# Performance work log

Measured on AMD Instinct MI355X. Metric: run time of the kernel, lower is better.

The kernel has to match this reference:

```python
import jax, jax.numpy as jnp
import numpy as np

BS, GRID, LSTM_H, CNN_C, PROJ = 256, 49, 512, 2048, 512


def setup_inputs() -> dict:
    key = jax.random.key(0)
    ks = jax.random.split(key, 7)
    s = lambda fan_in: 1.0 / np.sqrt(fan_in)
    return {
        "lstm_hidden": jax.random.normal(ks[0], (BS, LSTM_H), jnp.float32),
        "cnn_feat": jax.random.normal(ks[1], (BS, GRID, CNN_C), jnp.float32),
        "W_lstm": jax.random.normal(ks[2], (PROJ, LSTM_H), jnp.float32) * s(LSTM_H),
        "b_lstm": jax.random.normal(ks[3], (PROJ,), jnp.float32) * s(LSTM_H),
        "W_cnn": jax.random.normal(ks[4], (PROJ, CNN_C), jnp.float32) * s(CNN_C),
        "b_cnn": jax.random.normal(ks[5], (PROJ,), jnp.float32) * s(CNN_C),
        "w_attn": jax.random.normal(ks[6], (1, PROJ), jnp.float32) * s(PROJ),
    }


def reference(lstm_hidden, cnn_feat, W_lstm, b_lstm, W_cnn, b_cnn, w_attn):
    # H computed once (original loop recomputes it per grid, identically)
    H = lstm_hidden @ W_lstm.T + b_lstm                       # (bs, P)
    V = jnp.einsum("bgc,pc->bgp", cnn_feat, W_cnn) + b_cnn    # (bs, G, P)
    z = jnp.tanh(H[:, None, :] + V) @ w_attn[0]               # (bs, G)
    bs, G = z.shape
    # Faithful to torch: cat over grids along dim 0 -> (G*bs,), then view(bs, G)
    z_scrambled = jnp.swapaxes(z, 0, 1).reshape(bs, G)
    return jax.nn.softmax(z_scrambled, axis=1)
```

## Files before the change

kernel.cpp:

```cpp
#include <hip/hip_runtime.h>
#include <math.h>

#define BSZ    256
#define GRID_N 49
#define LSTMH  512
#define CNN_C  2048
#define PROJ   512
#define KAUG   2560
#define M_TOT  12544
#define MT     64
#define NT     128
#define BK     64
#define KTILES (KAUG / BK)
#define NBLK   ((M_TOT / MT) * (PROJ / NT))

typedef short bf16x8 __attribute__((ext_vector_type(8)));
typedef float f32x4  __attribute__((ext_vector_type(4)));

static __device__ __forceinline__ unsigned short bf16_rne(float f) {
    unsigned int u = __float_as_uint(f);
    u = u + 0x7FFFu + ((u >> 16) & 1u);
    return (unsigned short)(u >> 16);
}
static __device__ __forceinline__ uint4 pack8f(const float* f) {
    uint4 o;
    o.x = (unsigned int)bf16_rne(f[0]) | ((unsigned int)bf16_rne(f[1]) << 16);
    o.y = (unsigned int)bf16_rne(f[2]) | ((unsigned int)bf16_rne(f[3]) << 16);
    o.z = (unsigned int)bf16_rne(f[4]) | ((unsigned int)bf16_rne(f[5]) << 16);
    o.w = (unsigned int)bf16_rne(f[6]) | ((unsigned int)bf16_rne(f[7]) << 16);
    return o;
}
static __device__ __forceinline__ float tanh_fast(float x) {
    float e = __expf(2.f * x);
    return 1.f - 2.f / (e + 1.f);
}
static __device__ __forceinline__ void glds16(const void* g, void* l) {
    __builtin_amdgcn_global_load_lds(
        (const __attribute__((address_space(1))) unsigned int*)g,
        (__attribute__((address_space(3))) unsigned int*)l, 16, 0, 0);
}

__global__ __launch_bounds__(256) void prep_w(const float* __restrict__ Wc,
                                              const float* __restrict__ Wl,
                                              unsigned short* __restrict__ wsW) {
    int c  = blockIdx.x * 256 + threadIdx.x;
    int p  = c / 320;
    int kc = (c % 320) * 8;
    const float* src = (kc < CNN_C) ? (Wc + (size_t)p * CNN_C + kc)
                                    : (Wl + (size_t)p * LSTMH + (kc - CNN_C));
    float f[8];
    *(float4*)&f[0] = ((const float4*)src)[0];
    *(float4*)&f[4] = ((const float4*)src)[1];
    *(uint4*)(wsW + (size_t)p * KAUG + kc) = pack8f(f);
}

template <bool WS>
__global__ __launch_bounds__(256, 4) void gemm_k(
    const float* __restrict__ lstm, const float* __restrict__ cnn,
    const float* __restrict__ Wc,   const float* __restrict__ Wl,
    const float* __restrict__ bl,   const float* __restrict__ bc,
    const float* __restrict__ wat,  const unsigned short* __restrict__ wsW,
    float* __restrict__ out)
{
    __shared__ unsigned short Ash[MT][BK];
    __shared__ unsigned short Bsh[NT][BK];
    __shared__ float zp[4][MT];

    const int t   = threadIdx.x;
    const int w   = t >> 6;
    const int l   = t & 63;
    const int q   = l >> 4;
    const int r16 = l & 15;

    const int bid = (int)blockIdx.x;
    const int swz = (bid & 7) * (NBLK / 8) + (bid >> 3);
    const int m0 = (swz >> 2) * MT;
    const int n0 = (swz & 3) * NT;

    const int ra  = t >> 2;
    const int ca0 = t & 3;
    const int sa  = ra & 7;
    const int grow = m0 + ra;
    const int ab   = grow / 49;
    const int ag   = grow - ab * 49;
    const float* cnnb  = cnn + ((size_t)ab * GRID_N + ag) * CNN_C;
    const float* lstmb = lstm + (size_t)ab * LSTMH;

    f32x4 acc[4][2];
    #pragma unroll
    for (int mt = 0; mt < 4; ++mt)
        #pragma unroll
        for (int nt = 0; nt < 2; ++nt)
            acc[mt][nt] = (f32x4){0.f, 0.f, 0.f, 0.f};

    float4 fa0, fa1, fa2, fa3;

    auto a_load = [&](int k0) {
        const float* s = (k0 < CNN_C) ? (cnnb + k0) : (lstmb + (k0 - CNN_C));
        const float4* p0 = (const float4*)(s + ca0 * 8);
        const float4* p1 = (const float4*)(s + (ca0 + 4) * 8);
        fa0 = p0[0]; fa1 = p0[1];
        fa2 = p1[0]; fa3 = p1[1];
    };
    auto a_write = [&]() {
        float f[8];
        *(float4*)&f[0] = fa0; *(float4*)&f[4] = fa1;
        *(uint4*)&Ash[ra][(ca0 ^ sa) * 8] = pack8f(f);
        *(float4*)&f[0] = fa2; *(float4*)&f[4] = fa3;
        *(uint4*)&Ash[ra][((ca0 + 4) ^ sa) * 8] = pack8f(f);
    };
    auto b_stage = [&](int k0) {
        if constexpr (WS) {
            const int rsub = l >> 3;
            const int cg   = (l & 7) ^ rsub;
            #pragma unroll
            for (int j = 0; j < 4; ++j) {
                const int rowb = w * 32 + j * 8;
                const unsigned short* g =
                    wsW + (size_t)(n0 + rowb + rsub) * KAUG + k0 + cg * 8;
                glds16(g, &Bsh[rowb][0]);
            }
        } else {
            const int rb = t >> 1;
            const int hb = t & 1;
            const float* s = (k0 < CNN_C) ? (Wc + (size_t)(n0 + rb) * CNN_C + k0)
                                          : (Wl + (size_t)(n0 + rb) * LSTMH + (k0 - CNN_C));
            const int sw = rb & 7;
            #pragma unroll
            for (int c = 0; c < 4; ++c) {
                const int cc = hb * 4 + c;
                float f[8];
                *(float4*)&f[0] = ((const float4*)(s + cc * 8))[0];
                *(float4*)&f[4] = ((const float4*)(s + cc * 8))[1];
                *(uint4*)&Bsh[rb][(cc ^ sw) * 8] = pack8f(f);
            }
        }
    };

    a_load(0);
    a_write();
    b_stage(0);

    for (int kt = 0; kt < KTILES; ++kt) {
        __syncthreads();
        const bool more = (kt + 1 < KTILES);
        if (more) a_load((kt + 1) * BK);
        #pragma unroll
        for (int ks = 0; ks < 2; ++ks) {
            const int cp = ((ks * 4 + q) ^ (r16 & 7)) * 8;
            bf16x8 af[4], bfr[2];
            #pragma unroll
            for (int mt = 0; mt < 4; ++mt)
                af[mt] = *(const bf16x8*)&Ash[mt * 16 + r16][cp];
            #pragma unroll
            for (int nt = 0; nt < 2; ++nt)
                bfr[nt] = *(const bf16x8*)&Bsh[w * 32 + nt * 16 + r16][cp];
            #pragma unroll
            for (int mt = 0; mt < 4; ++mt)
                #pragma unroll
                for (int nt = 0; nt < 2; ++nt)
                    acc[mt][nt] = __builtin_amdgcn_mfma_f32_16x16x32_bf16(
                        af[mt], bfr[nt], acc[mt][nt], 0, 0, 0);
        }
        __syncthreads();
        if (more) { a_write(); b_stage((kt + 1) * BK); }
    }

    float part[4][4];
    #pragma unroll
    for (int mt = 0; mt < 4; ++mt)
        #pragma unroll
        for (int rr = 0; rr < 4; ++rr) part[mt][rr] = 0.f;
    #pragma unroll
    for (int nt = 0; nt < 2; ++nt) {
        const int p = n0 + w * 32 + nt * 16 + r16;
        const float bb = bl[p] + bc[p];
        const float wa = wat[p];
        #pragma unroll
        for (int mt = 0; mt < 4; ++mt)
            #pragma unroll
            for (int rr = 0; rr < 4; ++rr)
                part[mt][rr] += tanh_fast(acc[mt][nt][rr] + bb) * wa;
    }
    #pragma unroll
    for (int mt = 0; mt < 4; ++mt)
        #pragma unroll
        for (int rr = 0; rr < 4; ++rr) {
            float v = part[mt][rr];
            v += __shfl_xor(v, 1);
            v += __shfl_xor(v, 2);
            v += __shfl_xor(v, 4);
            v += __shfl_xor(v, 8);
            if (r16 == 0) zp[w][mt * 16 + q * 4 + rr] = v;
        }
    __syncthreads();
    if (t < MT) {
        const float v = zp[0][t] + zp[1][t] + zp[2][t] + zp[3][t];
        const int row = m0 + t;
        const int b2  = row / 49;
        const int g2  = row - b2 * 49;
        atomicAdd(&out[g2 * BSZ + b2], v);
    }
}

__global__ __launch_bounds__(64) void softmax_rows(float* __restrict__ out)
{
    const int i = blockIdx.x;
    const int j = threadIdx.x;
    float x = (j < GRID_N) ? out[i * GRID_N + j] : -1e30f;
    float m = x;
    #pragma unroll
    for (int off = 32; off > 0; off >>= 1) m = fmaxf(m, __shfl_xor(m, off));
    float e = (j < GRID_N) ? __expf(x - m) : 0.f;
    float s = e;
    #pragma unroll
    for (int off = 32; off > 0; off >>= 1) s += __shfl_xor(s, off);
    if (j < GRID_N) out[i * GRID_N + j] = e / s;
}

extern "C" void kernel_launch(void* const* d_in, const int* in_sizes, int n_in,
                              void* d_out, int out_size, void* d_ws, size_t ws_size,
                              hipStream_t stream)
{
    const float* lstm = (const float*)d_in[0];
    const float* cnn  = (const float*)d_in[1];
    const float* Wl   = (const float*)d_in[2];
    const float* bl   = (const float*)d_in[3];
    const float* Wc   = (const float*)d_in[4];
    const float* bc   = (const float*)d_in[5];
    const float* wat  = (const float*)d_in[6];
    float* out = (float*)d_out;

    hipMemsetAsync(out, 0, (size_t)out_size * sizeof(float), stream);

    const size_t wneed = (size_t)PROJ * KAUG * sizeof(unsigned short);
    if (ws_size >= wneed) {
        unsigned short* wsW = (unsigned short*)d_ws;
        prep_w<<<dim3(640), dim3(256), 0, stream>>>(Wc, Wl, wsW);
        gemm_k<true><<<dim3(NBLK), dim3(256), 0, stream>>>(lstm, cnn, Wc, Wl, bl, bc, wat, wsW, out);
    } else {
        gemm_k<false><<<dim3(NBLK), dim3(256), 0, stream>>>(lstm, cnn, Wc, Wl, bl, bc, wat, nullptr, out);
    }
    softmax_rows<<<dim3(BSZ), dim3(64), 0, stream>>>(out);
}
```

Baseline: 246.6 us.

## Pre-convert activations to bf16 and use a 128x128 double-buffered direct-to-LDS GEMM

A new prep kernel converts cnn_feat and lstm_hidden to bf16 in workspace alongside the weights, and also zeroes the output, which removes the separate memset. A new GEMM kernel uses 128x128 tiles with double-buffered LDS filled through global_load_lds for both operands. Register-staged fp32 loads and per-tile conversion inside the main loop go away, and each block gets more reuse per tile. The cost is an extra full pass over the 100MB activation tensor, which is read, written as bf16 and read again, and the new path only runs if the workspace is large enough.

```diff
diff --git a/kernel.cpp b/kernel.cpp
--- a/kernel.cpp
+++ b/kernel.cpp
@@ -8,11 +8,22 @@
 #define PROJ   512
 #define KAUG   2560
 #define M_TOT  12544
+#define BK     64
+#define KTILES (KAUG / BK)
+
 #define MT     64
 #define NT     128
-#define BK     64
-#define KTILES (KAUG / BK)
 #define NBLK   ((M_TOT / MT) * (PROJ / NT))
+
+#define MT2    128
+#define NT2    128
+#define NBLK2  ((M_TOT / MT2) * (PROJ / NT2))
+
+#define ACHUNKS (M_TOT * CNN_C / 8)
+#define LCHUNKS (BSZ * LSTMH / 8)
+#define ABLK    ((ACHUNKS + LCHUNKS) / 256)
+#define WBLK    640
+#define PBLK    (ABLK + WBLK)
 
 typedef short bf16x8 __attribute__((ext_vector_type(8)));
 typedef float f32x4  __attribute__((ext_vector_type(4)));
@@ -38,6 +49,161 @@
     __builtin_amdgcn_global_load_lds(
         (const __attribute__((address_space(1))) unsigned int*)g,
         (__attribute__((address_space(3))) unsigned int*)l, 16, 0, 0);
+}
+
+__global__ __launch_bounds__(256) void prep_all(
+    const float* __restrict__ cnn, const float* __restrict__ lstm,
+    const float* __restrict__ Wc,  const float* __restrict__ Wl,
+    unsigned short* __restrict__ wsW, unsigned short* __restrict__ wsA,
+    unsigned short* __restrict__ wsL, float* __restrict__ out)
+{
+    const int bid = blockIdx.x, t = threadIdx.x;
+    if (bid < 49) out[bid * 256 + t] = 0.f;
+    float f[8];
+    if (bid < ABLK) {
+        const int c = bid * 256 + t;
+        const float* src; unsigned short* dst;
+        if (c < ACHUNKS) { src = cnn  + (size_t)c * 8; dst = wsA + (size_t)c * 8; }
+        else { const int c2 = c - ACHUNKS; src = lstm + (size_t)c2 * 8; dst = wsL + (size_t)c2 * 8; }
+        *(float4*)&f[0] = ((const float4*)src)[0];
+        *(float4*)&f[4] = ((const float4*)src)[1];
+        *(uint4*)dst = pack8f(f);
+    } else {
+        const int c  = (bid - ABLK) * 256 + t;
+        const int p  = c / 320;
+        const int kc = (c % 320) * 8;
+        const float* src = (kc < CNN_C) ? (Wc + (size_t)p * CNN_C + kc)
+                                        : (Wl + (size_t)p * LSTMH + (kc - CNN_C));
+        *(float4*)&f[0] = ((const float4*)src)[0];
+        *(float4*)&f[4] = ((const float4*)src)[1];
+        *(uint4*)(wsW + (size_t)p * KAUG + kc) = pack8f(f);
+    }
+}
+
+__global__ __launch_bounds__(256, 2) void gemm2(
+    const unsigned short* __restrict__ wsW, const unsigned short* __restrict__ wsA,
+    const unsigned short* __restrict__ wsL,
+    const float* __restrict__ bl, const float* __restrict__ bc,
+    const float* __restrict__ wat, float* __restrict__ out)
+{
+    __shared__ unsigned short Ab[2][MT2][BK];
+    __shared__ unsigned short Bb[2][NT2][BK];
+
+    const int t   = threadIdx.x;
+    const int w   = t >> 6;
+    const int l   = t & 63;
+    const int q   = l >> 4;
+    const int r16 = l & 15;
+    const int wr  = w >> 1;
+    const int wc  = w & 1;
+
+    const int bid = (int)blockIdx.x;
+    const int swz = (bid & 7) * (NBLK2 / 8) + (bid >> 3);
+    const int m0  = (swz >> 2) * MT2;
+    const int n0  = (swz & 3) * NT2;
+
+    const int srow = l >> 3;
+    const int cg   = (l & 7) ^ srow;
+
+    auto stage = [&](int kt, int bufi) {
+        const int k0 = kt * BK;
+        #pragma unroll
+        for (int jj = 0; jj < 4; ++jj) {
+            const int rowb = w * 32 + jj * 8;
+            const unsigned short* g = wsW + (size_t)(n0 + rowb + srow) * KAUG + k0 + cg * 8;
+            glds16(g, &Bb[bufi][rowb][0]);
+        }
+        if (k0 < CNN_C) {
+            #pragma unroll
+            for (int jj = 0; jj < 4; ++jj) {
+                const int rowa = w * 32 + jj * 8;
+                const unsigned short* g = wsA + (size_t)(m0 + rowa + srow) * CNN_C + k0 + cg * 8;
+                glds16(g, &Ab[bufi][rowa][0]);
+            }
+        } else {
+            const int k0l = k0 - CNN_C;
+            #pragma unroll
+            for (int jj = 0; jj < 4; ++jj) {
+                const int rowa = w * 32 + jj * 8;
+                const int rg   = m0 + rowa + srow;
+                const unsigned short* g = wsL + (size_t)(rg / 49) * LSTMH + k0l + cg * 8;
+                glds16(g, &Ab[bufi][rowa][0]);
+            }
+        }
+    };
+
+    f32x4 acc[4][4];
+    #pragma unroll
+    for (int mt = 0; mt < 4; ++mt)
+        #pragma unroll
+        for (int nt = 0; nt < 4; ++nt)
+            acc[mt][nt] = (f32x4){0.f, 0.f, 0.f, 0.f};
+
+    stage(0, 0);
+    asm volatile("s_waitcnt vmcnt(0)" ::: "memory");
+    __builtin_amdgcn_s_barrier();
+
+    int cur = 0;
+    for (int kt = 0; kt < KTILES; ++kt) {
+        if (kt + 1 < KTILES) stage(kt + 1, cur ^ 1);
+        #pragma unroll
+        for (int ks = 0; ks < 2; ++ks) {
+            const int cp = ((ks * 4 + q) ^ (r16 & 7)) * 8;
+            bf16x8 af[4], bfr[4];
+            #pragma unroll
+            for (int mt = 0; mt < 4; ++mt)
+                af[mt] = *(const bf16x8*)&Ab[cur][wr * 64 + mt * 16 + r16][cp];
+            #pragma unroll
+            for (int nt = 0; nt < 4; ++nt)
+                bfr[nt] = *(const bf16x8*)&Bb[cur][wc * 64 + nt * 16 + r16][cp];
+            #pragma unroll
+            for (int mt = 0; mt < 4; ++mt)
+                #pragma unroll
+                for (int nt = 0; nt < 4; ++nt)
+                    acc[mt][nt] = __builtin_amdgcn_mfma_f32_16x16x32_bf16(
+                        af[mt], bfr[nt], acc[mt][nt], 0, 0, 0);
+        }
+        asm volatile("s_waitcnt vmcnt(0)" ::: "memory");
+        __builtin_amdgcn_s_barrier();
+        cur ^= 1;
+    }
+
+    float* zpf = (float*)&Ab[0][0][0];
+    float part[4][4];
+    #pragma unroll
+    for (int mt = 0; mt < 4; ++mt)
+        #pragma unroll
+        for (int rr = 0; rr < 4; ++rr) part[mt][rr] = 0.f;
+    #pragma unroll
+    for (int nt = 0; nt < 4; ++nt) {
+        const int p = n0 + wc * 64 + nt * 16 + r16;
+        const float bb = bl[p] + bc[p];
+        const float wa = wat[p];
+        #pragma unroll
+        for (int mt = 0; mt < 4; ++mt)
+            #pragma unroll
+            for (int rr = 0; rr < 4; ++rr)
+                part[mt][rr] += tanh_fast(acc[mt][nt][rr] + bb) * wa;
+    }
+    #pragma unroll
+    for (int mt = 0; mt < 4; ++mt)
+        #pragma unroll
+        for (int rr = 0; rr < 4; ++rr) {
+            float v = part[mt][rr];
+            v += __shfl_xor(v, 1);
+            v += __shfl_xor(v, 2);
+            v += __shfl_xor(v, 4);
+            v += __shfl_xor(v, 8);
+            if (r16 == 0) zpf[wc * MT2 + wr * 64 + mt * 16 + q * 4 + rr] = v;
+        }
+    __syncthreads();
+    if (t < MT2) {
+        const float v = zpf[t] + zpf[MT2 + t];
+        const int row = m0 + t;
+        const int b2  = row / 49;
+        const int g2  = row - b2 * 49;
+        atomicAdd(&out[g2 * BSZ + b2], v);
+    }
 }
 
 __global__ __launch_bounds__(256) void prep_w(const float* __restrict__ Wc,
@@ -231,14 +397,23 @@
     const float* wat  = (const float*)d_in[6];
     float* out = (float*)d_out;
 
-    hipMemsetAsync(out, 0, (size_t)out_size * sizeof(float), stream);
-
-    const size_t wneed = (size_t)PROJ * KAUG * sizeof(unsigned short);
-    if (ws_size >= wneed) {
+    const size_t szW = (size_t)PROJ * KAUG * sizeof(unsigned short);
+    const size_t szA = (size_t)M_TOT * CNN_C * sizeof(unsigned short);
+    const size_t szL = (size_t)BSZ * LSTMH * sizeof(unsigned short);
+
+    if (ws_size >= szW + szA + szL) {
         unsigned short* wsW = (unsigned short*)d_ws;
-        prep_w<<<dim3(640), dim3(256), 0, stream>>>(Wc, Wl, wsW);
+        unsigned short* wsA = wsW + (size_t)PROJ * KAUG;
+        unsigned short* wsL = wsA + (size_t)M_TOT * CNN_C;
+        prep_all<<<dim3(PBLK), dim3(256), 0, stream>>>(cnn, lstm, Wc, Wl, wsW, wsA, wsL, out);
+        gemm2<<<dim3(NBLK2), dim3(256), 0, stream>>>(wsW, wsA, wsL, bl, bc, wat, out);
+    } else if (ws_size >= szW) {
+        hipMemsetAsync(out, 0, (size_t)out_size * sizeof(float), stream);
+        unsigned short* wsW = (unsigned short*)d_ws;
+        prep_w<<<dim3(WBLK), dim3(256), 0, stream>>>(Wc, Wl, wsW);
         gemm_k<true><<<dim3(NBLK), dim3(256), 0, stream>>>(lstm, cnn, Wc, Wl, bl, bc, wat, wsW, out);
     } else {
+        hipMemsetAsync(out, 0, (size_t)out_size * sizeof(float), stream);
         gemm_k<false><<<dim3(NBLK), dim3(256), 0, stream>>>(lstm, cnn, Wc, Wl, bl, bc, wat, nullptr, out);
     }
     softmax_rows<<<dim3(BSZ), dim3(64), 0, stream>>>(out);
```

Result: faster. 218.0 us (-11.6%).
